# Performance work log

Hardware: AMD Instinct MI355X
Metric: run time of the kernel (lower is better)

Reference implementation:

```python
import jax, jax.numpy as jnp
import numpy as np

NV = 6890          # SMPL vertex count
NF = 13776         # SMPL face count
N_CHUNKS = 10
EUCL_THRES = 0.02  # euclthres
WN_THRES = 0.99    # exterior if winding number <= 0.99


def _winding_numbers(points, tris):
    """Generalized winding numbers of `points` [m,3] w.r.t. triangle soup `tris` [f,3,3].
    Solid angle per (point, triangle) via the van-Oosterom/Strackee atan2 formula."""
    r = tris[None, :, :, :] - points[:, None, None, :]   # [m,f,3,3]
    ra, rb, rc = r[:, :, 0, :], r[:, :, 1, :], r[:, :, 2, :]
    la = jnp.linalg.norm(ra, axis=-1)
    lb = jnp.linalg.norm(rb, axis=-1)
    lc = jnp.linalg.norm(rc, axis=-1)
    det = jnp.einsum('mfi,mfi->mf', ra, jnp.cross(rb, rc))
    denom = (la * lb * lc
             + jnp.sum(ra * rb, -1) * lc
             + jnp.sum(rb * rc, -1) * la
             + jnp.sum(rc * ra, -1) * lb)
    omega = 2.0 * jnp.arctan2(det, denom)                # [m,f]
    return jnp.sum(omega, axis=-1) / (4.0 * jnp.pi)      # [m]


def setup_inputs() -> dict:
    key = jax.random.key(0)
    k1, k2, k3 = jax.random.split(key, 3)
    vertices = jax.random.normal(k1, (1, NV, 3), dtype=jnp.float32)
    faces = jax.random.randint(k2, (NF, 3), 0, NV)
    # geodesic-distance >= geothres mask: symmetric, False on the diagonal
    gm = jax.random.uniform(k3, (NV, NV)) > 0.3
    gm = gm & gm.T
    gm = gm.at[jnp.arange(NV), jnp.arange(NV)].set(False)
    return {"vertices": vertices, "faces": faces, "geomask": gm}


def reference(vertices, faces, geomask):
    # triangles(vertices): gather face corner coordinates  [NF,3,3] (bs=1)
    tris = vertices[0][faces]
    # get_intersection_mask: chunked winding numbers, exterior = wn <= 0.99
    pts = vertices[0].reshape(N_CHUNKS, NV // N_CHUNKS, 3)
    wn = jax.lax.map(lambda p: _winding_numbers(p, tris), pts).reshape(NV)
    exterior = (wn <= WN_THRES)[None, :]                 # [1,NV] bool
    # batch_pairwise_dist (squared=False)
    x = vertices[0]                                      # [NV,3]
    sq = jnp.sum(x * x, axis=-1)
    d2 = sq[:, None] + sq[None, :] - 2.0 * (x @ x.T)
    v2v = jnp.sqrt(jnp.maximum(d2, 0.0))                 # [NV,NV]
    # mask geodesically-near pairs with inf, take per-vertex min over dim 1
    masked = jnp.where(geomask, v2v, jnp.inf)
    idx = jnp.argmin(masked, axis=0)                     # argmin over rows for each column
    v2v_min = v2v[jnp.arange(NV), idx][None, :]          # gather along dim 2 (symmetric)
    incontact = v2v_min < EUCL_THRES
    return v2v_min, incontact, exterior
```

## Files before the change

kernel.cpp:

```cpp
#include <hip/hip_runtime.h>
#include <math.h>

#define NV 6890
#define NF 13776
#define NVPAD 6912
#define NFPAD 13824
#define NPBLK 27
#define TCH 64
#define TPC 216
#define V2V_BLOCKS 1723
#define WN_BLOCKS (NPBLK*TCH)
#define WN_THRES 0.99
#define EUCL_THRES 0.02f

#define WS_TRIS_OFF   64
#define WS_X4_OFF     (64 + NFPAD*48)
#define WS_PART_OFF   (WS_X4_OFF + NVPAD*16)

__global__ __launch_bounds__(256) void prep_kernel(
    const float* __restrict__ verts, const int* __restrict__ faces,
    const unsigned char* __restrict__ gm_bytes,
    float* __restrict__ tris12, float* __restrict__ x4, int* __restrict__ flag)
{
    int t = blockIdx.x * 256 + threadIdx.x;

    if (t < NFPAD) {
        float* o = tris12 + (size_t)t * 12;
        if (t < NF) {
            int ia = faces[t*3+0], ib = faces[t*3+1], ic = faces[t*3+2];
            o[0]  = verts[ia*3+0]; o[1]  = verts[ia*3+1]; o[2]  = verts[ia*3+2]; o[3]  = 0.f;
            o[4]  = verts[ib*3+0]; o[5]  = verts[ib*3+1]; o[6]  = verts[ib*3+2]; o[7]  = 0.f;
            o[8]  = verts[ic*3+0]; o[9]  = verts[ic*3+1]; o[10] = verts[ic*3+2]; o[11] = 0.f;
        } else {
            #pragma unroll
            for (int q = 0; q < 12; ++q) o[q] = 0.f;
        }
    }
    if (t < NVPAD) {
        if (t < NV) {
            float x = verts[t*3+0], y = verts[t*3+1], z = verts[t*3+2];
            x4[t*4+0] = x; x4[t*4+1] = y; x4[t*4+2] = z;
            x4[t*4+3] = (x*x + y*y) + z*z;
        } else {
            x4[t*4+0] = 0.f; x4[t*4+1] = 0.f; x4[t*4+2] = 0.f; x4[t*4+3] = 0.f;
        }
    }
    if (blockIdx.x == 0 && threadIdx.x < 64) {
        int lane = threadIdx.x;
        bool any3F = false, anyNZmod = false;
        for (int k = 0; k < 64; ++k) {
            int off = lane * 64 + k;
            unsigned char b = gm_bytes[off];
            if ((off & 3) == 3 && (b == 0x3F || b == 0xBF)) any3F = true;
            if ((off & 3) != 0 && b != 0) anyNZmod = true;
        }
        unsigned long long m3F = __ballot(any3F);
        unsigned long long mNZ = __ballot(anyNZmod);
        if (lane == 0) {
            *flag = m3F ? 2 : (mNZ ? 0 : 1);
        }
    }
}

__device__ __forceinline__ float fast_atan2f(float y, float x)
{
    float ay = __builtin_fabsf(y), ax = __builtin_fabsf(x);
    float mx = fmaxf(ax, ay);
    float mn = fminf(ax, ay);
    float r  = __builtin_amdgcn_rcpf(fmaxf(mx, 1e-37f));
    float t  = mn * r;
    float s  = t * t;
    float u  =              0.00282363896258175373077393f;
    u = fmaf(u, s, -0.0159569028764963150024414f);
    u = fmaf(u, s,  0.0425049886107444763183594f);
    u = fmaf(u, s, -0.0748900920152664184570312f);
    u = fmaf(u, s,  0.106347933411598205566406f);
    u = fmaf(u, s, -0.142027363181114196777344f);
    u = fmaf(u, s,  0.199926957488059997558594f);
    u = fmaf(u, s, -0.333331018686294555664062f);
    float p = fmaf(s * u, t, t);
    p = (ay > ax)  ? (1.5707963267948966f - p) : p;
    p = (x < 0.0f) ? (3.14159265358979323846f - p) : p;
    return copysignf(p, y);
}

__global__ __launch_bounds__(256) void fused_kernel(
    const float4* __restrict__ tris12, const float4* __restrict__ x4,
    float* __restrict__ partials,
    const void* __restrict__ gm, const int* __restrict__ flag_p,
    float* __restrict__ out)
{
    if (blockIdx.x < V2V_BLOCKS) {
        int w = threadIdx.x >> 6;
        int lane = threadIdx.x & 63;
        int j = blockIdx.x * 4 + w;
        if (j >= NV) return;

        int flag = *flag_p;
        float4 vj = x4[j];
        float m = INFINITY;

#define V2V_BODY(GTEST)                                            \
        {                                                          \
            int i0 = 0;                                            \
            for (; i0 + 64 <= NV; i0 += 64) {                      \
                int i = i0 + lane;                                 \
                bool g = (GTEST);                                  \
                float4 vi = x4[i];                                 \
                float dot = (vi.x*vj.x + vi.y*vj.y) + vi.z*vj.z;   \
                float d2  = vi.w + vj.w - 2.0f*dot;                \
                m = fminf(m, g ? d2 : INFINITY);                   \
            }                                                      \
            int i = i0 + lane;                                     \
            if (i < NV) {                                          \
                bool g = (GTEST);                                  \
                float4 vi = x4[i];                                 \
                float dot = (vi.x*vj.x + vi.y*vj.y) + vi.z*vj.z;   \
                float d2  = vi.w + vj.w - 2.0f*dot;                \
                m = fminf(m, g ? d2 : INFINITY);                   \
            }                                                      \
        }

        if (flag == 0) {
            const unsigned char* row = (const unsigned char*)gm + (size_t)j * NV;
            V2V_BODY(row[i] != 0)
        } else if (flag == 1) {
            const int* row = (const int*)gm + (size_t)j * NV;
            V2V_BODY(row[i] != 0)
        } else {
            const float* row = (const float*)gm + (size_t)j * NV;
            V2V_BODY(row[i] != 0.0f)
        }
#undef V2V_BODY

        #pragma unroll
        for (int k = 32; k > 0; k >>= 1)
            m = fminf(m, __shfl_xor(m, k, 64));
        if (lane == 0) {
            float d = __builtin_amdgcn_sqrtf(fmaxf(m, 0.f));
            out[j] = d;
            out[NV + j] = (d < EUCL_THRES) ? 1.f : 0.f;
        }
    } else {
        int wnb = blockIdx.x - V2V_BLOCKS;
        int tc = wnb / NPBLK;
        int pb = wnb - tc * NPBLK;
        int pt = pb * 256 + threadIdx.x;

        float4 P = x4[pt];
        float px = P.x, py = P.y, pz = P.z;
        const float4* __restrict__ T = tris12 + (size_t)tc * (TPC * 3);

        double acc = 0.0;
        for (int kk = 0; kk < TPC; kk += 4) {
            float s4 = 0.f;
            #pragma unroll
            for (int u = 0; u < 4; ++u) {
                const float4* Tk = T + 3 * (kk + u);
                float4 A = Tk[0];
                float4 B = Tk[1];
                float4 C = Tk[2];
                float ax = A.x - px, ay = A.y - py, az = A.z - pz;
                float bx = B.x - px, by = B.y - py, bz = B.z - pz;
                float cx = C.x - px, cy = C.y - py, cz = C.z - pz;

                float la = __builtin_amdgcn_sqrtf((ax*ax + ay*ay) + az*az);
                float lb = __builtin_amdgcn_sqrtf((bx*bx + by*by) + bz*bz);
                float lc = __builtin_amdgcn_sqrtf((cx*cx + cy*cy) + cz*cz);

                float ux = by*cz - bz*cy;
                float uy = bz*cx - bx*cz;
                float uz = bx*cy - by*cx;
                float det = (ax*ux + ay*uy) + az*uz;

                float dab = (ax*bx + ay*by) + az*bz;
                float dbc = (bx*cx + by*cy) + bz*cz;
                float dca = (cx*ax + cy*ay) + cz*az;

                float denom = la*lb*lc + dab*lc + dbc*la + dca*lb;

                s4 += fast_atan2f(det, denom);
            }
            acc += (double)s4;
        }

        partials[(size_t)tc * NVPAD + pt] = (float)acc;
    }
}

__global__ __launch_bounds__(256) void wn_reduce_kernel(
    const float* __restrict__ partials, float* __restrict__ out_exterior)
{
    int pt = blockIdx.x * 256 + threadIdx.x;
    if (pt >= NV) return;
    double s = 0.0;
    for (int t = 0; t < TCH; ++t) s += (double)partials[(size_t)t * NVPAD + pt];
    double wn = (2.0 * s) / 12.566370614359172953850573533118;
    out_exterior[pt] = (wn <= WN_THRES) ? 1.0f : 0.0f;
}

extern "C" void kernel_launch(void* const* d_in, const int* in_sizes, int n_in,
                              void* d_out, int out_size, void* d_ws, size_t ws_size,
                              hipStream_t stream)
{
    const float* verts = (const float*)d_in[0];
    const int*   faces = (const int*)d_in[1];
    const void*  gm    = d_in[2];
    float* out = (float*)d_out;
    char* ws = (char*)d_ws;

    int*   flag     = (int*)ws;
    float* tris12   = (float*)(ws + WS_TRIS_OFF);
    float* x4       = (float*)(ws + WS_X4_OFF);
    float* partials = (float*)(ws + WS_PART_OFF);

    prep_kernel<<<NFPAD / 256, 256, 0, stream>>>(
        verts, faces, (const unsigned char*)gm, tris12, x4, flag);

    fused_kernel<<<V2V_BLOCKS + WN_BLOCKS, 256, 0, stream>>>(
        (const float4*)tris12, (const float4*)x4, partials, gm, flag, out);

    wn_reduce_kernel<<<NPBLK, 256, 0, stream>>>(partials, out + 2 * NV);
}
```

Before: 501.9 us.

## Register-block two query points per thread and prefetch triangles, schedule WN blocks first

Each winding-number thread now handles two query points (pt and pt+HALF), so every triangle load is reused for two solid-angle evaluations. The triangles for the next iteration are loaded into registers ahead of use as a software prefetch. The WN blocks are moved ahead of the v2v blocks in the fused grid so the compute-heavy part is dispatched first. This raises register pressure and halves WN thread-level parallelism, which could lower occupancy.

```diff
diff --git a/kernel.cpp b/kernel.cpp
--- a/kernel.cpp
+++ b/kernel.cpp
@@ -5,11 +5,13 @@
 #define NF 13776
 #define NVPAD 6912
 #define NFPAD 13824
-#define NPBLK 27
+#define HALF 3456
+#define PBLK 14
 #define TCH 64
 #define TPC 216
+#define WN_BLOCKS (PBLK*TCH)
 #define V2V_BLOCKS 1723
-#define WN_BLOCKS (NPBLK*TCH)
+#define RED_BLOCKS 27
 #define WN_THRES 0.99
 #define EUCL_THRES 0.02f
 
@@ -84,16 +86,73 @@
     return copysignf(p, y);
 }
 
+#define TRI_OMEGA(A, B, C, PX, PY, PZ, S)                                 \
+    {                                                                     \
+        float ax = A.x - PX, ay = A.y - PY, az = A.z - PZ;                \
+        float bx = B.x - PX, by = B.y - PY, bz = B.z - PZ;                \
+        float cx = C.x - PX, cy = C.y - PY, cz = C.z - PZ;                \
+        float la = __builtin_amdgcn_sqrtf((ax*ax + ay*ay) + az*az);       \
+        float lb = __builtin_amdgcn_sqrtf((bx*bx + by*by) + bz*bz);       \
+        float lc = __builtin_amdgcn_sqrtf((cx*cx + cy*cy) + cz*cz);       \
+        float ux = by*cz - bz*cy;                                         \
+        float uy = bz*cx - bx*cz;                                         \
+        float uz = bx*cy - by*cx;                                         \
+        float det = (ax*ux + ay*uy) + az*uz;                              \
+        float dab = (ax*bx + ay*by) + az*bz;                              \
+        float dbc = (bx*cx + by*cy) + bz*cz;                              \
+        float dca = (cx*ax + cy*ay) + cz*az;                              \
+        float denom = la*lb*lc + dab*lc + dbc*la + dca*lb;                \
+        S += fast_atan2f(det, denom);                                     \
+    }
+
 __global__ __launch_bounds__(256) void fused_kernel(
     const float4* __restrict__ tris12, const float4* __restrict__ x4,
     float* __restrict__ partials,
     const void* __restrict__ gm, const int* __restrict__ flag_p,
     float* __restrict__ out)
 {
-    if (blockIdx.x < V2V_BLOCKS) {
+    if (blockIdx.x < WN_BLOCKS) {
+        int tc = blockIdx.x / PBLK;
+        int pb = blockIdx.x - tc * PBLK;
+        int pt = pb * 256 + threadIdx.x;
+        if (pt >= HALF) return;
+        int p1i = pt + HALF;
+
+        float4 P0 = x4[pt];
+        float4 P1 = x4[p1i];
+        float px0 = P0.x, py0 = P0.y, pz0 = P0.z;
+        float px1 = P1.x, py1 = P1.y, pz1 = P1.z;
+
+        const float4* __restrict__ T = tris12 + (size_t)tc * (TPC * 3);
+
+        float4 A0 = T[0], B0 = T[1], C0 = T[2];
+        float4 A1 = T[3], B1 = T[4], C1 = T[5];
+        double acc0 = 0.0, acc1 = 0.0;
+
+        for (int kk = 0; kk < TPC; kk += 2) {
+            int n0 = 3 * min(kk + 2, TPC - 1);
+            int n1 = 3 * min(kk + 3, TPC - 1);
+            float s0 = 0.f, s1 = 0.f;
+
+            TRI_OMEGA(A0, B0, C0, px0, py0, pz0, s0);
+            TRI_OMEGA(A0, B0, C0, px1, py1, pz1, s1);
+            A0 = T[n0]; B0 = T[n0 + 1]; C0 = T[n0 + 2];
+
+            TRI_OMEGA(A1, B1, C1, px0, py0, pz0, s0);
+            TRI_OMEGA(A1, B1, C1, px1, py1, pz1, s1);
+            A1 = T[n1]; B1 = T[n1 + 1]; C1 = T[n1 + 2];
+
+            acc0 += (double)s0;
+            acc1 += (double)s1;
+        }
+
+        partials[(size_t)tc * NVPAD + pt]  = (float)acc0;
+        partials[(size_t)tc * NVPAD + p1i] = (float)acc1;
+    } else {
+        int bid = blockIdx.x - WN_BLOCKS;
         int w = threadIdx.x >> 6;
         int lane = threadIdx.x & 63;
-        int j = blockIdx.x * 4 + w;
+        int j = bid * 4 + w;
         if (j >= NV) return;
 
         int flag = *flag_p;
@@ -141,50 +200,6 @@
             out[j] = d;
             out[NV + j] = (d < EUCL_THRES) ? 1.f : 0.f;
         }
-    } else {
-        int wnb = blockIdx.x - V2V_BLOCKS;
-        int tc = wnb / NPBLK;
-        int pb = wnb - tc * NPBLK;
-        int pt = pb * 256 + threadIdx.x;
-
-        float4 P = x4[pt];
-        float px = P.x, py = P.y, pz = P.z;
-        const float4* __restrict__ T = tris12 + (size_t)tc * (TPC * 3);
-
-        double acc = 0.0;
-        for (int kk = 0; kk < TPC; kk += 4) {
-            float s4 = 0.f;
-            #pragma unroll
-            for (int u = 0; u < 4; ++u) {
-                const float4* Tk = T + 3 * (kk + u);
-                float4 A = Tk[0];
-                float4 B = Tk[1];
-                float4 C = Tk[2];
-                float ax = A.x - px, ay = A.y - py, az = A.z - pz;
-                float bx = B.x - px, by = B.y - py, bz = B.z - pz;
-                float cx = C.x - px, cy = C.y - py, cz = C.z - pz;
-
-                float la = __builtin_amdgcn_sqrtf((ax*ax + ay*ay) + az*az);
-                float lb = __builtin_amdgcn_sqrtf((bx*bx + by*by) + bz*bz);
-                float lc = __builtin_amdgcn_sqrtf((cx*cx + cy*cy) + cz*cz);
-
-                float ux = by*cz - bz*cy;
-                float uy = bz*cx - bx*cz;
-                float uz = bx*cy - by*cx;
-                float det = (ax*ux + ay*uy) + az*uz;
-
-                float dab = (ax*bx + ay*by) + az*bz;
-                float dbc = (bx*cx + by*cy) + bz*cz;
-                float dca = (cx*ax + cy*ay) + cz*az;
-
-                float denom = la*lb*lc + dab*lc + dbc*la + dca*lb;
-
-                s4 += fast_atan2f(det, denom);
-            }
-            acc += (double)s4;
-        }
-
-        partials[(size_t)tc * NVPAD + pt] = (float)acc;
     }
 }
 
@@ -217,8 +232,8 @@
     prep_kernel<<<NFPAD / 256, 256, 0, stream>>>(
         verts, faces, (const unsigned char*)gm, tris12, x4, flag);
 
-    fused_kernel<<<V2V_BLOCKS + WN_BLOCKS, 256, 0, stream>>>(
+    fused_kernel<<<WN_BLOCKS + V2V_BLOCKS, 256, 0, stream>>>(
         (const float4*)tris12, (const float4*)x4, partials, gm, flag, out);
 
-    wn_reduce_kernel<<<NPBLK, 256, 0, stream>>>(partials, out + 2 * NV);
-}
+    wn_reduce_kernel<<<RED_BLOCKS, 256, 0, stream>>>(partials, out + 2 * NV);
+}
```

After: 441.4 us. -12.0%, faster.
